# Optimization experiments

Measured on AMD Instinct MI355X. Metric: run time of the kernel, lower is better.

Reference implementation:

```python
import jax, jax.numpy as jnp
import numpy as np

NEG_SLOPE = 0.2

def _linear(x, w, b):
    return x @ w.T + b

def _encode(samples, w1, b1, w2, b2, lnw, lnb):
    t = samples[:, :, 0:1] / 10000.0
    a = samples[:, :, 1:2] / 20000.0
    x = jnp.concatenate([t, a], axis=2)
    x = jax.nn.relu(_linear(x, w1, b1))
    x = jax.nn.relu(_linear(x, w2, b2))
    mu = x.mean(-1, keepdims=True)
    var = x.var(-1, keepdims=True)
    x = (x - mu) / jnp.sqrt(var + 1e-5) * lnw + lnb
    mask = (jnp.abs(samples).sum(2) > 0).astype(x.dtype)
    denom = jnp.clip(mask.sum(1, keepdims=True), 1e-6, None)
    return (x * mask[:, :, None]).sum(1) / denom

def _gatv2(x, src, dst, edge_attr, wl, bl, wr, br, we, att, bias, H, C):
    N = x.shape[0]
    # PyG add_self_loops with fill_value='mean': self-loop edge_attr = mean of incoming edge_attr per node
    ones = jnp.ones((edge_attr.shape[0],), x.dtype)
    cnt = jax.ops.segment_sum(ones, dst, num_segments=N)
    ea_mean = jax.ops.segment_sum(edge_attr, dst, num_segments=N) / jnp.maximum(cnt, 1.0)[:, None]
    loop = jnp.arange(N, dtype=src.dtype)
    src2 = jnp.concatenate([src, loop])
    dst2 = jnp.concatenate([dst, loop])
    ea2 = jnp.concatenate([edge_attr, ea_mean], axis=0)
    xl = _linear(x, wl, bl).reshape(N, H, C)   # source transform
    xr = _linear(x, wr, br).reshape(N, H, C)   # target transform
    ee = (ea2 @ we.T).reshape(-1, H, C)        # edge conditioning (no bias in PyG lin_edge)
    z = xl[src2] + xr[dst2] + ee               # [E2, H, C]
    z = jnp.where(z > 0, z, NEG_SLOPE * z)     # leaky_relu(0.2)
    logit = jnp.einsum('ehc,hc->eh', z, att)   # [E2, H]
    m = jax.ops.segment_max(logit, dst2, num_segments=N)
    a = jnp.exp(logit - m[dst2])
    denom = jax.ops.segment_sum(a, dst2, num_segments=N)
    a = a / (denom[dst2] + 1e-16)              # PyG softmax eps
    out = jax.ops.segment_sum(xl[src2] * a[:, :, None], dst2, num_segments=N)
    return out.mean(axis=1) + bias             # concat=False -> head mean, then bias


def setup_inputs():
    key = jax.random.key(0)
    ks = jax.random.split(key, 32)
    N, S, E = 30000, 50, 400000
    ED, GD, H = 32, 64, 4
    def w(k, shape, s=0.1):
        return jax.random.normal(k, shape, jnp.float32) * s
    return {
        "samples": jax.random.normal(ks[0], (N, S, 2), jnp.float32),
        "edge_index": jax.random.randint(ks[1], (2, E), 0, N, dtype=jnp.int32),
        "edge_attr": jax.random.normal(ks[2], (E, 1), jnp.float32),
        "enc_fc1_w": w(ks[3], (ED, 2)), "enc_fc1_b": w(ks[4], (ED,)),
        "enc_fc2_w": w(ks[5], (ED, ED)), "enc_fc2_b": w(ks[6], (ED,)),
        "enc_ln_w": jnp.ones((ED,), jnp.float32), "enc_ln_b": jnp.zeros((ED,), jnp.float32),
        "g1_wl": w(ks[7], (H * GD, ED)), "g1_bl": w(ks[8], (H * GD,)),
        "g1_wr": w(ks[9], (H * GD, ED)), "g1_br": w(ks[10], (H * GD,)),
        "g1_we": w(ks[11], (H * GD, 1)), "g1_att": w(ks[12], (H, GD)),
        "g1_bias": w(ks[13], (GD,)),
        "g2_wl": w(ks[14], (H * GD, GD)), "g2_bl": w(ks[15], (H * GD,)),
        "g2_wr": w(ks[16], (H * GD, GD)), "g2_br": w(ks[17], (H * GD,)),
        "g2_we": w(ks[18], (H * GD, 1)), "g2_att": w(ks[19], (H, GD)),
        "g2_bias": w(ks[20], (GD,)),
        "head_w": w(ks[21], (2, GD)), "head_b": w(ks[22], (2,)),
    }


def reference(samples, edge_index, edge_attr,
              enc_fc1_w, enc_fc1_b, enc_fc2_w, enc_fc2_b, enc_ln_w, enc_ln_b,
              g1_wl, g1_bl, g1_wr, g1_br, g1_we, g1_att, g1_bias,
              g2_wl, g2_bl, g2_wr, g2_br, g2_we, g2_att, g2_bias,
              head_w, head_b):
    H, GD = 4, 64
    src, dst = edge_index[0], edge_index[1]
    x = _encode(samples, enc_fc1_w, enc_fc1_b, enc_fc2_w, enc_fc2_b, enc_ln_w, enc_ln_b)
    x = jax.nn.relu(_gatv2(x, src, dst, edge_attr, g1_wl, g1_bl, g1_wr, g1_br, g1_we, g1_att, g1_bias, H, GD))
    x = jax.nn.relu(_gatv2(x, src, dst, edge_attr, g2_wl, g2_bl, g2_wr, g2_br, g2_we, g2_att, g2_bias, H, GD))
    out = _linear(x, head_w, head_b)
    Q = out[:, 0]
    logv = jnp.clip(out[:, 1], -5.0, 10.0)
    return (Q, logv)
```

## Files before the change

### kernel.cpp

```cpp
#include <hip/hip_runtime.h>
#include <hip/hip_fp16.h>
#include <math.h>

#define NSAMP 50
#define ED 32
#define GD 64
#define NH 4
#define STRIDE 40

typedef _Float16 f16;
typedef f16 f16x4 __attribute__((ext_vector_type(4)));
typedef f16 f16x8 __attribute__((ext_vector_type(8)));
typedef float f32x4 __attribute__((ext_vector_type(4)));
typedef f16 h2v __attribute__((ext_vector_type(2)));

__device__ __forceinline__ float red16(float x) {
    int t;
    t = __builtin_amdgcn_update_dpp(0, __float_as_int(x), 0x121, 0xF, 0xF, false);
    x += __int_as_float(t);
    t = __builtin_amdgcn_update_dpp(0, __float_as_int(x), 0x122, 0xF, 0xF, false);
    x += __int_as_float(t);
    t = __builtin_amdgcn_update_dpp(0, __float_as_int(x), 0x124, 0xF, 0xF, false);
    x += __int_as_float(t);
    t = __builtin_amdgcn_update_dpp(0, __float_as_int(x), 0x128, 0xF, 0xF, false);
    x += __int_as_float(t);
    return x;
}

__global__ __launch_bounds__(256) void encode_mfma_kernel(
    const float* __restrict__ samples,
    const float* __restrict__ w1, const float* __restrict__ b1,
    const float* __restrict__ w2, const float* __restrict__ b2,
    const float* __restrict__ lnw, const float* __restrict__ lnb,
    __half* __restrict__ x0h, int N)
{
    int lane = threadIdx.x & 63, wv = threadIdx.x >> 6;
    int n = blockIdx.x * 4 + wv;
    if (n >= N) return;
    int cl = lane & 15, kg = lane >> 4;

    f16x8 af[2];
#pragma unroll
    for (int ct = 0; ct < 2; ct++) {
        const float* wrow = w2 + (size_t)(ct * 16 + cl) * ED;
        float4 lo4 = *(const float4*)(wrow + kg * 4);
        float4 hi4 = *(const float4*)(wrow + 16 + kg * 4);
        f16x8 ah;
        ah[0] = (f16)lo4.x; ah[1] = (f16)lo4.y; ah[2] = (f16)lo4.z; ah[3] = (f16)lo4.w;
        ah[4] = (f16)hi4.x; ah[5] = (f16)hi4.y; ah[6] = (f16)hi4.z; ah[7] = (f16)hi4.w;
        af[ct] = ah;
    }
    float4 bias0 = *(const float4*)(b2 + kg * 4);
    float4 bias1 = *(const float4*)(b2 + 16 + kg * 4);
    float4 wp0 = *(const float4*)(w1 + 8 * kg);
    float4 wp1 = *(const float4*)(w1 + 8 * kg + 4);
    float4 wp2 = *(const float4*)(w1 + 32 + 8 * kg);
    float4 wp3 = *(const float4*)(w1 + 32 + 8 * kg + 4);
    float4 b1lo = *(const float4*)(b1 + 4 * kg);
    float4 b1hi = *(const float4*)(b1 + 16 + 4 * kg);
    const float w1a[8] = {wp0.x, wp0.z, wp1.x, wp1.z, wp2.x, wp2.z, wp3.x, wp3.z};
    const float w1b[8] = {wp0.y, wp0.w, wp1.y, wp1.w, wp2.y, wp2.w, wp3.y, wp3.w};
    const float b1v[8] = {b1lo.x, b1lo.y, b1lo.z, b1lo.w, b1hi.x, b1hi.y, b1hi.z, b1hi.w};

    float P1a[4] = {0.f, 0.f, 0.f, 0.f};
    float P1b[4] = {0.f, 0.f, 0.f, 0.f};
    float P2 = 0.f, W = 0.f;

#pragma unroll
    for (int t = 0; t < 4; t++) {
        int slot = t * 16 + cl;
        float rt = 0.f, ra = 0.f;
        if (slot < NSAMP) {
            float2 v = *(const float2*)(samples + ((size_t)n * NSAMP + slot) * 2);
            rt = v.x; ra = v.y;
        }
        float msk = (fabsf(rt) + fabsf(ra)) > 0.f ? 1.f : 0.f;
        float xi0 = rt * 1e-4f, xi1 = ra * 5e-5f;

        f16x8 bf_;
#pragma unroll
        for (int i = 0; i < 8; i++) {
            float h1 = fmaxf(fmaf(w1a[i], xi0, fmaf(w1b[i], xi1, b1v[i])), 0.f);
            bf_[i] = (f16)h1;
        }

        f32x4 c0 = {bias0.x, bias0.y, bias0.z, bias0.w};
        f32x4 c1 = {bias1.x, bias1.y, bias1.z, bias1.w};
        c0 = __builtin_amdgcn_mfma_f32_16x16x32_f16(af[0], bf_, c0, 0, 0, 0);
        c1 = __builtin_amdgcn_mfma_f32_16x16x32_f16(af[1], bf_, c1, 0, 0, 0);

        float s = 0.f, q = 0.f;
#pragma unroll
        for (int r = 0; r < 4; r++) {
            float h0 = fmaxf(c0[r], 0.f), h1v = fmaxf(c1[r], 0.f);
            c0[r] = h0; c1[r] = h1v;
            s += h0 + h1v;
            q = fmaf(h0, h0, fmaf(h1v, h1v, q));
        }
        s += __shfl_xor(s, 16); s += __shfl_xor(s, 32);
        q += __shfl_xor(q, 16); q += __shfl_xor(q, 32);

        float mu  = s * (1.f / 32.f);
        float var = fmaf(-mu, mu, q * (1.f / 32.f));
        float inv = 1.f / sqrtf(var + 1e-5f);
        float a   = inv * msk;
        P2 = fmaf(-mu, a, P2);
        W += msk;
#pragma unroll
        for (int r = 0; r < 4; r++) {
            P1a[r] = fmaf(a, c0[r], P1a[r]);
            P1b[r] = fmaf(a, c1[r], P1b[r]);
        }
    }

#pragma unroll
    for (int off = 1; off <= 8; off <<= 1) {
#pragma unroll
        for (int r = 0; r < 4; r++) {
            P1a[r] += __shfl_xor(P1a[r], off);
            P1b[r] += __shfl_xor(P1b[r], off);
        }
        P2 += __shfl_xor(P2, off);
        W  += __shfl_xor(W, off);
    }
    if (cl == 0) {
        float rr = 1.f / fmaxf(W, 1e-6f);
        float4 lw0 = *(const float4*)(lnw + kg * 4);
        float4 lb0 = *(const float4*)(lnb + kg * 4);
        float4 lw1 = *(const float4*)(lnw + 16 + kg * 4);
        float4 lb1 = *(const float4*)(lnb + 16 + kg * 4);
        float o0 = (lw0.x * (P1a[0] + P2) + lb0.x * W) * rr;
        float o1 = (lw0.y * (P1a[1] + P2) + lb0.y * W) * rr;
        float o2 = (lw0.z * (P1a[2] + P2) + lb0.z * W) * rr;
        float o3 = (lw0.w * (P1a[3] + P2) + lb0.w * W) * rr;
        float o4 = (lw1.x * (P1b[0] + P2) + lb1.x * W) * rr;
        float o5 = (lw1.y * (P1b[1] + P2) + lb1.y * W) * rr;
        float o6 = (lw1.z * (P1b[2] + P2) + lb1.z * W) * rr;
        float o7 = (lw1.w * (P1b[3] + P2) + lb1.w * W) * rr;
        __half2 h0 = __floats2half2_rn(o0, o1), h1 = __floats2half2_rn(o2, o3);
        __half2 h2 = __floats2half2_rn(o4, o5), h3 = __floats2half2_rn(o6, o7);
        *(uint2*)(x0h + (size_t)n * ED + kg * 4) =
            make_uint2(*(unsigned*)&h0, *(unsigned*)&h1);
        *(uint2*)(x0h + (size_t)n * ED + 16 + kg * 4) =
            make_uint2(*(unsigned*)&h2, *(unsigned*)&h3);
    }
}

__global__ void build_csr_kernel(const int* __restrict__ src, const int* __restrict__ dst,
                                 const float* __restrict__ ea,
                                 int* __restrict__ cnt, unsigned* __restrict__ csru, int E) {
    int e = blockIdx.x * blockDim.x + threadIdx.x;
    if (e >= E) return;
    int d = dst[e];
    int slot = atomicAdd(&cnt[d], 1);
    if (slot < STRIDE)
        csru[(size_t)d * STRIDE + slot] =
            ((unsigned)src[e] << 16) | (unsigned)__half_as_ushort(__float2half_rn(ea[e]));
}

template <int D>
__global__ __launch_bounds__(256) void xlxr_mfma_kernel(
    const __half* __restrict__ xh,
    const float* __restrict__ wl, const float* __restrict__ bl,
    const float* __restrict__ wr, const float* __restrict__ br,
    __half* __restrict__ xl, __half* __restrict__ xr,
    int nTiles, int tilesPerBlock)
{
    int lane = threadIdx.x & 63, wv = threadIdx.x >> 6;
    int cl = lane & 15, kg = lane >> 4;
    bool isR = blockIdx.y != 0;
    const float* wp = isR ? wr : wl;
    const float* bp = isR ? br : bl;
    __half* outp = isR ? xr : xl;
    int colbase = wv * 64;

    const int KS = D / 32;
    f16x8 bf[4][2];
    float bias_[4];
#pragma unroll
    for (int ct = 0; ct < 4; ct++) {
        int col = colbase + ct * 16 + cl;
        bias_[ct] = bp[col];
        const float* wrow = wp + (size_t)col * D;
#pragma unroll
        for (int ks = 0; ks < KS; ks++) {
            float4 lo = *(const float4*)(wrow + ks * 32 + kg * 4);
            float4 hi = *(const float4*)(wrow + ks * 32 + kg * 4 + 16);
            f16x8 bb;
            bb[0] = (f16)lo.x; bb[1] = (f16)lo.y; bb[2] = (f16)lo.z; bb[3] = (f16)lo.w;
            bb[4] = (f16)hi.x; bb[5] = (f16)hi.y; bb[6] = (f16)hi.z; bb[7] = (f16)hi.w;
            bf[ct][ks] = bb;
        }
    }

    int t0 = blockIdx.x * tilesPerBlock;
    int t1 = min(t0 + tilesPerBlock, nTiles);
    for (int t = t0; t < t1; ++t) {
        const __half* rp = xh + ((size_t)(t * 16 + cl)) * D;
        f16x8 a[2];
#pragma unroll
        for (int ks = 0; ks < KS; ks++) {
            f16x4 alo = *(const f16x4*)(rp + ks * 32 + kg * 4);
            f16x4 ahi = *(const f16x4*)(rp + ks * 32 + kg * 4 + 16);
            a[ks] = __builtin_shufflevector(alo, ahi, 0, 1, 2, 3, 4, 5, 6, 7);
        }
        int r0 = t * 16 + kg * 4;
#pragma unroll
        for (int ct = 0; ct < 4; ct++) {
            f32x4 c = {bias_[ct], bias_[ct], bias_[ct], bias_[ct]};
#pragma unroll
            for (int ks = 0; ks < KS; ks++)
                c = __builtin_amdgcn_mfma_f32_16x16x32_f16(a[ks], bf[ct][ks], c, 0, 0, 0);
            int col = colbase + ct * 16 + cl;
#pragma unroll
            for (int i = 0; i < 4; i++)
                outp[(size_t)(r0 + i) * 256 + col] = __float2half(c[i]);
        }
    }
}

template <bool FINAL>
__global__ __launch_bounds__(64) void gat_kernel(
    const __half* __restrict__ xl, const __half* __restrict__ xr,
    const int* __restrict__ cnt_arr, const unsigned* __restrict__ csru,
    const float* __restrict__ we, const float* __restrict__ att,
    const float* __restrict__ bias,
    const float* __restrict__ hw, const float* __restrict__ hb,
    void* __restrict__ xout, int N)
{
    int lane = threadIdx.x & 63;
    int n = blockIdx.x;
    const char* xlb = (const char*)xl;
    const uint2* xrh = (const uint2*)xr;
    uint2 xrp = xrh[(size_t)n * 64 + lane];
    h2v xr01 = __builtin_bit_cast(h2v, xrp.x);
    h2v xr23 = __builtin_bit_cast(h2v, xrp.y);
    float4 wev = ((const float4*)we)[lane];
    float4 atv = ((const float4*)att)[lane];
    const float L2E = 1.44269504088896340736f;

    h2v we01, we23, a601, a623, a401, a423;
    we01[0] = (f16)wev.x; we01[1] = (f16)wev.y;
    we23[0] = (f16)wev.z; we23[1] = (f16)wev.w;
    a601[0] = (f16)(atv.x * (0.6f * L2E)); a601[1] = (f16)(atv.y * (0.6f * L2E));
    a623[0] = (f16)(atv.z * (0.6f * L2E)); a623[1] = (f16)(atv.w * (0.6f * L2E));
    a401[0] = (f16)(atv.x * (0.4f * L2E)); a401[1] = (f16)(atv.y * (0.4f * L2E));
    a423[0] = (f16)(atv.z * (0.4f * L2E)); a423[1] = (f16)(atv.w * (0.4f * L2E));

    int cnt_s = __builtin_amdgcn_readfirstlane(cnt_arr[n]);
    int cc = min(cnt_s, STRIDE);

    unsigned upk = (unsigned)n << 16;
    if (lane < cc) upk = csru[(size_t)n * STRIDE + lane];

    float veaf = __half2float(__ushort_as_half((unsigned short)(upk & 0xFFFFu)));
    float sea = veaf;
#pragma unroll
    for (int off = 1; off <= 32; off <<= 1) sea += __shfl_xor(sea, off);
    float eself = sea / fmaxf((float)cnt_s, 1.f);

    float S0 = 0.f, S1 = 0.f;
    float4 A0 = make_float4(0, 0, 0, 0), A1 = make_float4(0, 0, 0, 0);

    uint2 xA[4], xB[4];
    unsigned uA[4], uB[4];
    int laneoff = lane * 8;

    auto fetchg = [&](int k0, uint2* xv, unsigned* uv) {
#pragma unroll
        for (int c = 0; c < 4; ++c) {
            unsigned u = (unsigned)__builtin_amdgcn_readlane((int)upk, k0 + c);
            uv[c] = u;
            int off = (int)((u >> 16) << 9);
            xv[c] = *(const uint2*)(xlb + off + laneoff);
        }
    };
    auto edgeu = [&](uint2 xc, unsigned u, float& S, float4& A) {
        h2v x01 = __builtin_bit_cast(h2v, xc.x);
        h2v x23 = __builtin_bit_cast(h2v, xc.y);
        unsigned eb = (u & 0xFFFFu) * 0x10001u;
        h2v e2 = __builtin_bit_cast(h2v, eb);
        h2v z01 = e2 * we01 + (x01 + xr01);
        h2v z23 = e2 * we23 + (x23 + xr23);
        h2v az01 = __builtin_bit_cast(h2v, __builtin_bit_cast(int, z01) & 0x7FFF7FFF);
        h2v az23 = __builtin_bit_cast(h2v, __builtin_bit_cast(int, z23) & 0x7FFF7FFF);
        float part = __builtin_amdgcn_fdot2(a601, z01, 0.f, false);
        part = __builtin_amdgcn_fdot2(a623, z23, part, false);
        part = __builtin_amdgcn_fdot2(a401, az01, part, false);
        part = __builtin_amdgcn_fdot2(a423, az23, part, false);
        part = red16(part);
        float p = exp2f(part);
        S += p;
        A.x = fmaf(p, (float)x01[0], A.x);
        A.y = fmaf(p, (float)x01[1], A.y);
        A.z = fmaf(p, (float)x23[0], A.z);
        A.w = fmaf(p, (float)x23[1], A.w);
    };
    auto procg = [&](const uint2* xv, const unsigned* uv) {
        edgeu(xv[0], uv[0], S0, A0);
        edgeu(xv[1], uv[1], S1, A1);
        edgeu(xv[2], uv[2], S0, A0);
        edgeu(xv[3], uv[3], S1, A1);
    };

    uint2 xself = *(const uint2*)(xlb + ((size_t)n << 9) + laneoff);

    int fullg = cc >> 2, rem = cc & 3;
    if (fullg > 0) {
        fetchg(0, xA, uA);
        int g = 0;
        while (true) {
            if (g + 1 < fullg) fetchg((g + 1) * 4, xB, uB);
            procg(xA, uA);
            if (++g >= fullg) break;
            if (g + 1 < fullg) fetchg((g + 1) * 4, xA, uA);
            procg(xB, uB);
            if (++g >= fullg) break;
        }
    }
    for (int k = fullg * 4; k < cc; ++k) {
        unsigned u = (unsigned)__builtin_amdgcn_readlane((int)upk, k);
        int off = (int)((u >> 16) << 9);
        uint2 xc = *(const uint2*)(xlb + off + laneoff);
        edgeu(xc, u, S0, A0);
    }
    {
        h2v e2 = __builtin_bit_cast(h2v, __builtin_amdgcn_cvt_pkrtz(eself, eself));
        h2v x01 = __builtin_bit_cast(h2v, xself.x);
        h2v x23 = __builtin_bit_cast(h2v, xself.y);
        h2v z01 = e2 * we01 + (x01 + xr01);
        h2v z23 = e2 * we23 + (x23 + xr23);
        h2v az01 = __builtin_bit_cast(h2v, __builtin_bit_cast(int, z01) & 0x7FFF7FFF);
        h2v az23 = __builtin_bit_cast(h2v, __builtin_bit_cast(int, z23) & 0x7FFF7FFF);
        float part = __builtin_amdgcn_fdot2(a601, z01, 0.f, false);
        part = __builtin_amdgcn_fdot2(a623, z23, part, false);
        part = __builtin_amdgcn_fdot2(a401, az01, part, false);
        part = __builtin_amdgcn_fdot2(a423, az23, part, false);
        part = red16(part);
        float p = exp2f(part);
        S1 += p;
        A1.x = fmaf(p, (float)x01[0], A1.x);
        A1.y = fmaf(p, (float)x01[1], A1.y);
        A1.z = fmaf(p, (float)x23[0], A1.z);
        A1.w = fmaf(p, (float)x23[1], A1.w);
    }

    float S = S0 + S1;
    float4 A = make_float4(A0.x + A1.x, A0.y + A1.y, A0.z + A1.z, A0.w + A1.w);

    float inv = 1.f / S;
    float ox = A.x * inv, oy = A.y * inv, oz = A.z * inv, ow = A.w * inv;
    ox += __shfl_xor(ox, 16); ox += __shfl_xor(ox, 32);
    oy += __shfl_xor(oy, 16); oy += __shfl_xor(oy, 32);
    oz += __shfl_xor(oz, 16); oz += __shfl_xor(oz, 32);
    ow += __shfl_xor(ow, 16); ow += __shfl_xor(ow, 32);
    if (lane < 16) {
        float4 bv = ((const float4*)bias)[lane];
        ox = fmaxf(fmaf(ox, 0.25f, bv.x), 0.f);
        oy = fmaxf(fmaf(oy, 0.25f, bv.y), 0.f);
        oz = fmaxf(fmaf(oz, 0.25f, bv.z), 0.f);
        ow = fmaxf(fmaf(ow, 0.25f, bv.w), 0.f);
        if (!FINAL) {
            __half2 h0 = __floats2half2_rn(ox, oy);
            __half2 h1 = __floats2half2_rn(oz, ow);
            uint2 pk = make_uint2(*(unsigned*)&h0, *(unsigned*)&h1);
            *(uint2*)((__half*)xout + (size_t)n * 64 + lane * 4) = pk;
        } else {
            float* outp = (float*)xout;
            int c0 = lane * 4;
            float q = ox * hw[c0] + oy * hw[c0 + 1] + oz * hw[c0 + 2] + ow * hw[c0 + 3];
            float v = ox * hw[64 + c0] + oy * hw[64 + c0 + 1] + oz * hw[64 + c0 + 2] + ow * hw[64 + c0 + 3];
            q += __shfl_xor(q, 1); q += __shfl_xor(q, 2); q += __shfl_xor(q, 4); q += __shfl_xor(q, 8);
            v += __shfl_xor(v, 1); v += __shfl_xor(v, 2); v += __shfl_xor(v, 4); v += __shfl_xor(v, 8);
            if (lane == 0) {
                outp[n]     = q + hb[0];
                outp[N + n] = fminf(fmaxf(v + hb[1], -5.f), 10.f);
            }
        }
    }
}

extern "C" void kernel_launch(void* const* d_in, const int* in_sizes, int n_in,
                              void* d_out, int out_size, void* d_ws, size_t ws_size,
                              hipStream_t stream)
{
    const float* samples    = (const float*)d_in[0];
    const int*   edge_index = (const int*)d_in[1];
    const float* edge_attr  = (const float*)d_in[2];
    const float* e_fc1_w = (const float*)d_in[3];
    const float* e_fc1_b = (const float*)d_in[4];
    const float* e_fc2_w = (const float*)d_in[5];
    const float* e_fc2_b = (const float*)d_in[6];
    const float* e_ln_w  = (const float*)d_in[7];
    const float* e_ln_b  = (const float*)d_in[8];
    const float* g1_wl  = (const float*)d_in[9];
    const float* g1_bl  = (const float*)d_in[10];
    const float* g1_wr  = (const float*)d_in[11];
    const float* g1_br  = (const float*)d_in[12];
    const float* g1_we  = (const float*)d_in[13];
    const float* g1_att = (const float*)d_in[14];
    const float* g1_bias= (const float*)d_in[15];
    const float* g2_wl  = (const float*)d_in[16];
    const float* g2_bl  = (const float*)d_in[17];
    const float* g2_wr  = (const float*)d_in[18];
    const float* g2_br  = (const float*)d_in[19];
    const float* g2_we  = (const float*)d_in[20];
    const float* g2_att = (const float*)d_in[21];
    const float* g2_bias= (const float*)d_in[22];
    const float* head_w = (const float*)d_in[23];
    const float* head_b = (const float*)d_in[24];

    const int N = in_sizes[0] / (NSAMP * 2);
    const int E = in_sizes[2];
    const int* src = edge_index;
    const int* dst = edge_index + E;

    char* p = (char*)d_ws;
    auto take = [&](size_t bytes) { char* r = p; p += (bytes + 255) & ~(size_t)255; return r; };
    int*      cnt  = (int*)take((size_t)N * 4);
    unsigned* csru = (unsigned*)take((size_t)N * STRIDE * 4);
    __half*   x0h  = (__half*)take((size_t)N * ED * 2);
    __half*   x1h  = (__half*)take((size_t)N * GD * 2);
    __half*   xl   = (__half*)take((size_t)N * NH * GD * 2);
    __half*   xr   = (__half*)take((size_t)N * NH * GD * 2);
    (void)ws_size; (void)n_in; (void)out_size;

    (void)hipMemsetAsync(cnt, 0, (size_t)N * 4, stream);

    encode_mfma_kernel<<<(N + 3) / 4, 256, 0, stream>>>(samples, e_fc1_w, e_fc1_b,
                                                        e_fc2_w, e_fc2_b,
                                                        e_ln_w, e_ln_b, x0h, N);
    build_csr_kernel<<<(E + 255) / 256, 256, 0, stream>>>(src, dst, edge_attr, cnt, csru, E);

    const int TPB = 5;
    int nTiles = N / 16;
    dim3 mgrid((nTiles + TPB - 1) / TPB, 2);

    xlxr_mfma_kernel<ED><<<mgrid, 256, 0, stream>>>(x0h, g1_wl, g1_bl, g1_wr, g1_br,
                                                    xl, xr, nTiles, TPB);
    gat_kernel<false><<<N, 64, 0, stream>>>(xl, xr, cnt, csru, g1_we, g1_att, g1_bias,
                                            nullptr, nullptr, x1h, N);
    xlxr_mfma_kernel<GD><<<mgrid, 256, 0, stream>>>(x1h, g2_wl, g2_bl, g2_wr, g2_br,
                                                    xl, xr, nTiles, TPB);
    gat_kernel<true><<<N, 64, 0, stream>>>(xl, xr, cnt, csru, g2_we, g2_att, g2_bias,
                                           head_w, head_b, d_out, N);
}
```

Measured before the change: 168.2 us.

## Batch four nodes per encoder wave, fold count memset into encoder, split GAT accumulators

The encoder kernel now has each wave process four nodes, reusing the weight fragments already loaded and interleaving their independent MFMA and shuffle chains for more instruction-level parallelism. The separate memset of the CSR count array is removed: the first threads of each encoder block zero their slice of counts before the CSR build kernel runs. The GAT edge loop spreads its softmax accumulators across four independent sets instead of two, shortening the dependent FMA chains. In exchange the encoder uses more registers and launches fewer blocks, and the tail of the node range is clamped so some nodes are recomputed.

```diff
diff --git a/kernel.cpp b/kernel.cpp
--- a/kernel.cpp
+++ b/kernel.cpp
@@ -7,6 +7,7 @@
 #define GD 64
 #define NH 4
 #define STRIDE 40
+#define ENN 4
 
 typedef _Float16 f16;
 typedef f16 f16x4 __attribute__((ext_vector_type(4)));
@@ -32,12 +33,22 @@
     const float* __restrict__ w1, const float* __restrict__ b1,
     const float* __restrict__ w2, const float* __restrict__ b2,
     const float* __restrict__ lnw, const float* __restrict__ lnb,
-    __half* __restrict__ x0h, int N)
+    __half* __restrict__ x0h, int* __restrict__ cnt, int N)
 {
+    {
+        int tid = threadIdx.x;
+        if (tid < 4 * ENN) {
+            int idx = blockIdx.x * 4 * ENN + tid;
+            if (idx < N) cnt[idx] = 0;
+        }
+    }
     int lane = threadIdx.x & 63, wv = threadIdx.x >> 6;
-    int n = blockIdx.x * 4 + wv;
-    if (n >= N) return;
+    int nb = blockIdx.x * 4 * ENN + wv * ENN;
+    if (nb >= N) return;
     int cl = lane & 15, kg = lane >> 4;
+    int nn[ENN];
+#pragma unroll
+    for (int j = 0; j < ENN; j++) nn[j] = min(nb + j, N - 1);
 
     f16x8 af[2];
 #pragma unroll
@@ -62,87 +73,123 @@
     const float w1b[8] = {wp0.y, wp0.w, wp1.y, wp1.w, wp2.y, wp2.w, wp3.y, wp3.w};
     const float b1v[8] = {b1lo.x, b1lo.y, b1lo.z, b1lo.w, b1hi.x, b1hi.y, b1hi.z, b1hi.w};
 
-    float P1a[4] = {0.f, 0.f, 0.f, 0.f};
-    float P1b[4] = {0.f, 0.f, 0.f, 0.f};
-    float P2 = 0.f, W = 0.f;
+    float P1a[ENN][4], P1b[ENN][4], P2[ENN], W[ENN];
+#pragma unroll
+    for (int j = 0; j < ENN; j++) {
+        P2[j] = 0.f; W[j] = 0.f;
+#pragma unroll
+        for (int r = 0; r < 4; r++) { P1a[j][r] = 0.f; P1b[j][r] = 0.f; }
+    }
 
 #pragma unroll
     for (int t = 0; t < 4; t++) {
         int slot = t * 16 + cl;
-        float rt = 0.f, ra = 0.f;
+        float rt[ENN], ra[ENN];
+#pragma unroll
+        for (int j = 0; j < ENN; j++) { rt[j] = 0.f; ra[j] = 0.f; }
         if (slot < NSAMP) {
-            float2 v = *(const float2*)(samples + ((size_t)n * NSAMP + slot) * 2);
-            rt = v.x; ra = v.y;
-        }
-        float msk = (fabsf(rt) + fabsf(ra)) > 0.f ? 1.f : 0.f;
-        float xi0 = rt * 1e-4f, xi1 = ra * 5e-5f;
-
-        f16x8 bf_;
-#pragma unroll
-        for (int i = 0; i < 8; i++) {
-            float h1 = fmaxf(fmaf(w1a[i], xi0, fmaf(w1b[i], xi1, b1v[i])), 0.f);
-            bf_[i] = (f16)h1;
-        }
-
-        f32x4 c0 = {bias0.x, bias0.y, bias0.z, bias0.w};
-        f32x4 c1 = {bias1.x, bias1.y, bias1.z, bias1.w};
-        c0 = __builtin_amdgcn_mfma_f32_16x16x32_f16(af[0], bf_, c0, 0, 0, 0);
-        c1 = __builtin_amdgcn_mfma_f32_16x16x32_f16(af[1], bf_, c1, 0, 0, 0);
-
-        float s = 0.f, q = 0.f;
-#pragma unroll
-        for (int r = 0; r < 4; r++) {
-            float h0 = fmaxf(c0[r], 0.f), h1v = fmaxf(c1[r], 0.f);
-            c0[r] = h0; c1[r] = h1v;
-            s += h0 + h1v;
-            q = fmaf(h0, h0, fmaf(h1v, h1v, q));
-        }
-        s += __shfl_xor(s, 16); s += __shfl_xor(s, 32);
-        q += __shfl_xor(q, 16); q += __shfl_xor(q, 32);
-
-        float mu  = s * (1.f / 32.f);
-        float var = fmaf(-mu, mu, q * (1.f / 32.f));
-        float inv = 1.f / sqrtf(var + 1e-5f);
-        float a   = inv * msk;
-        P2 = fmaf(-mu, a, P2);
-        W += msk;
-#pragma unroll
-        for (int r = 0; r < 4; r++) {
-            P1a[r] = fmaf(a, c0[r], P1a[r]);
-            P1b[r] = fmaf(a, c1[r], P1b[r]);
+#pragma unroll
+            for (int j = 0; j < ENN; j++) {
+                float2 v = *(const float2*)(samples + ((size_t)nn[j] * NSAMP + slot) * 2);
+                rt[j] = v.x; ra[j] = v.y;
+            }
+        }
+        f16x8 bf[ENN];
+        float msk[ENN];
+#pragma unroll
+        for (int j = 0; j < ENN; j++) {
+            msk[j] = (fabsf(rt[j]) + fabsf(ra[j])) > 0.f ? 1.f : 0.f;
+            float xi0 = rt[j] * 1e-4f, xi1 = ra[j] * 5e-5f;
+#pragma unroll
+            for (int i = 0; i < 8; i++) {
+                float h1 = fmaxf(fmaf(w1a[i], xi0, fmaf(w1b[i], xi1, b1v[i])), 0.f);
+                bf[j][i] = (f16)h1;
+            }
+        }
+
+        f32x4 c0[ENN], c1[ENN];
+#pragma unroll
+        for (int j = 0; j < ENN; j++) {
+            c0[j] = f32x4{bias0.x, bias0.y, bias0.z, bias0.w};
+            c1[j] = f32x4{bias1.x, bias1.y, bias1.z, bias1.w};
+        }
+#pragma unroll
+        for (int j = 0; j < ENN; j++)
+            c0[j] = __builtin_amdgcn_mfma_f32_16x16x32_f16(af[0], bf[j], c0[j], 0, 0, 0);
+#pragma unroll
+        for (int j = 0; j < ENN; j++)
+            c1[j] = __builtin_amdgcn_mfma_f32_16x16x32_f16(af[1], bf[j], c1[j], 0, 0, 0);
+
+        float s[ENN], q[ENN];
+#pragma unroll
+        for (int j = 0; j < ENN; j++) {
+            float ss = 0.f, qq = 0.f;
+#pragma unroll
+            for (int r = 0; r < 4; r++) {
+                float h0 = fmaxf(c0[j][r], 0.f), h1v = fmaxf(c1[j][r], 0.f);
+                c0[j][r] = h0; c1[j][r] = h1v;
+                ss += h0 + h1v;
+                qq = fmaf(h0, h0, fmaf(h1v, h1v, qq));
+            }
+            s[j] = ss; q[j] = qq;
+        }
+#pragma unroll
+        for (int j = 0; j < ENN; j++) { s[j] += __shfl_xor(s[j], 16); q[j] += __shfl_xor(q[j], 16); }
+#pragma unroll
+        for (int j = 0; j < ENN; j++) { s[j] += __shfl_xor(s[j], 32); q[j] += __shfl_xor(q[j], 32); }
+
+#pragma unroll
+        for (int j = 0; j < ENN; j++) {
+            float mu  = s[j] * (1.f / 32.f);
+            float var = fmaf(-mu, mu, q[j] * (1.f / 32.f));
+            float inv = 1.f / sqrtf(var + 1e-5f);
+            float a   = inv * msk[j];
+            P2[j] = fmaf(-mu, a, P2[j]);
+            W[j] += msk[j];
+#pragma unroll
+            for (int r = 0; r < 4; r++) {
+                P1a[j][r] = fmaf(a, c0[j][r], P1a[j][r]);
+                P1b[j][r] = fmaf(a, c1[j][r], P1b[j][r]);
+            }
         }
     }
 
 #pragma unroll
     for (int off = 1; off <= 8; off <<= 1) {
 #pragma unroll
-        for (int r = 0; r < 4; r++) {
-            P1a[r] += __shfl_xor(P1a[r], off);
-            P1b[r] += __shfl_xor(P1b[r], off);
-        }
-        P2 += __shfl_xor(P2, off);
-        W  += __shfl_xor(W, off);
+        for (int j = 0; j < ENN; j++) {
+#pragma unroll
+            for (int r = 0; r < 4; r++) {
+                P1a[j][r] += __shfl_xor(P1a[j][r], off);
+                P1b[j][r] += __shfl_xor(P1b[j][r], off);
+            }
+            P2[j] += __shfl_xor(P2[j], off);
+            W[j]  += __shfl_xor(W[j], off);
+        }
     }
     if (cl == 0) {
-        float rr = 1.f / fmaxf(W, 1e-6f);
         float4 lw0 = *(const float4*)(lnw + kg * 4);
         float4 lb0 = *(const float4*)(lnb + kg * 4);
         float4 lw1 = *(const float4*)(lnw + 16 + kg * 4);
         float4 lb1 = *(const float4*)(lnb + 16 + kg * 4);
-        float o0 = (lw0.x * (P1a[0] + P2) + lb0.x * W) * rr;
-        float o1 = (lw0.y * (P1a[1] + P2) + lb0.y * W) * rr;
-        float o2 = (lw0.z * (P1a[2] + P2) + lb0.z * W) * rr;
-        float o3 = (lw0.w * (P1a[3] + P2) + lb0.w * W) * rr;
-        float o4 = (lw1.x * (P1b[0] + P2) + lb1.x * W) * rr;
-        float o5 = (lw1.y * (P1b[1] + P2) + lb1.y * W) * rr;
-        float o6 = (lw1.z * (P1b[2] + P2) + lb1.z * W) * rr;
-        float o7 = (lw1.w * (P1b[3] + P2) + lb1.w * W) * rr;
-        __half2 h0 = __floats2half2_rn(o0, o1), h1 = __floats2half2_rn(o2, o3);
-        __half2 h2 = __floats2half2_rn(o4, o5), h3 = __floats2half2_rn(o6, o7);
-        *(uint2*)(x0h + (size_t)n * ED + kg * 4) =
-            make_uint2(*(unsigned*)&h0, *(unsigned*)&h1);
-        *(uint2*)(x0h + (size_t)n * ED + 16 + kg * 4) =
-            make_uint2(*(unsigned*)&h2, *(unsigned*)&h3);
+#pragma unroll
+        for (int j = 0; j < ENN; j++) {
+            float rr = 1.f / fmaxf(W[j], 1e-6f);
+            float o0 = (lw0.x * (P1a[j][0] + P2[j]) + lb0.x * W[j]) * rr;
+            float o1 = (lw0.y * (P1a[j][1] + P2[j]) + lb0.y * W[j]) * rr;
+            float o2 = (lw0.z * (P1a[j][2] + P2[j]) + lb0.z * W[j]) * rr;
+            float o3 = (lw0.w * (P1a[j][3] + P2[j]) + lb0.w * W[j]) * rr;
+            float o4 = (lw1.x * (P1b[j][0] + P2[j]) + lb1.x * W[j]) * rr;
+            float o5 = (lw1.y * (P1b[j][1] + P2[j]) + lb1.y * W[j]) * rr;
+            float o6 = (lw1.z * (P1b[j][2] + P2[j]) + lb1.z * W[j]) * rr;
+            float o7 = (lw1.w * (P1b[j][3] + P2[j]) + lb1.w * W[j]) * rr;
+            __half2 h0 = __floats2half2_rn(o0, o1), h1 = __floats2half2_rn(o2, o3);
+            __half2 h2 = __floats2half2_rn(o4, o5), h3 = __floats2half2_rn(o6, o7);
+            *(uint2*)(x0h + (size_t)nn[j] * ED + kg * 4) =
+                make_uint2(*(unsigned*)&h0, *(unsigned*)&h1);
+            *(uint2*)(x0h + (size_t)nn[j] * ED + 16 + kg * 4) =
+                make_uint2(*(unsigned*)&h2, *(unsigned*)&h3);
+        }
     }
 }
 
@@ -259,8 +306,9 @@
     for (int off = 1; off <= 32; off <<= 1) sea += __shfl_xor(sea, off);
     float eself = sea / fmaxf((float)cnt_s, 1.f);
 
-    float S0 = 0.f, S1 = 0.f;
+    float S0 = 0.f, S1 = 0.f, S2 = 0.f, S3 = 0.f;
     float4 A0 = make_float4(0, 0, 0, 0), A1 = make_float4(0, 0, 0, 0);
+    float4 A2 = make_float4(0, 0, 0, 0), A3 = make_float4(0, 0, 0, 0);
 
     uint2 xA[4], xB[4];
     unsigned uA[4], uB[4];
@@ -299,13 +347,13 @@
     auto procg = [&](const uint2* xv, const unsigned* uv) {
         edgeu(xv[0], uv[0], S0, A0);
         edgeu(xv[1], uv[1], S1, A1);
-        edgeu(xv[2], uv[2], S0, A0);
-        edgeu(xv[3], uv[3], S1, A1);
+        edgeu(xv[2], uv[2], S2, A2);
+        edgeu(xv[3], uv[3], S3, A3);
     };
 
     uint2 xself = *(const uint2*)(xlb + ((size_t)n << 9) + laneoff);
 
-    int fullg = cc >> 2, rem = cc & 3;
+    int fullg = cc >> 2;
     if (fullg > 0) {
         fetchg(0, xA, uA);
         int g = 0;
@@ -345,8 +393,12 @@
         A1.w = fmaf(p, (float)x23[1], A1.w);
     }
 
-    float S = S0 + S1;
-    float4 A = make_float4(A0.x + A1.x, A0.y + A1.y, A0.z + A1.z, A0.w + A1.w);
+    float S = (S0 + S1) + (S2 + S3);
+    float4 A;
+    A.x = (A0.x + A1.x) + (A2.x + A3.x);
+    A.y = (A0.y + A1.y) + (A2.y + A3.y);
+    A.z = (A0.z + A1.z) + (A2.z + A3.z);
+    A.w = (A0.w + A1.w) + (A2.w + A3.w);
 
     float inv = 1.f / S;
     float ox = A.x * inv, oy = A.y * inv, oz = A.z * inv, ow = A.w * inv;
@@ -425,11 +477,8 @@
     __half*   xr   = (__half*)take((size_t)N * NH * GD * 2);
     (void)ws_size; (void)n_in; (void)out_size;
 
-    (void)hipMemsetAsync(cnt, 0, (size_t)N * 4, stream);
-
-    encode_mfma_kernel<<<(N + 3) / 4, 256, 0, stream>>>(samples, e_fc1_w, e_fc1_b,
-                                                        e_fc2_w, e_fc2_b,
-                                                        e_ln_w, e_ln_b, x0h, N);
+    encode_mfma_kernel<<<(N + 4 * ENN - 1) / (4 * ENN), 256, 0, stream>>>(
+        samples, e_fc1_w, e_fc1_b, e_fc2_w, e_fc2_b, e_ln_w, e_ln_b, x0h, cnt, N);
     build_csr_kernel<<<(E + 255) / 256, 256, 0, stream>>>(src, dst, edge_attr, cnt, csru, E);
 
     const int TPB = 5;
```

Result: no change. 167.0 us (-0.7%).
